# Kernel optimization log

Hardware: AMD Instinct MI355X
Metric: run time of the kernel (lower is better)

The kernel has to match this reference:

```python
import jax, jax.numpy as jnp
import numpy as np

N, E, IN, H, D = 50000, 800000, 16, 4, 64


def _gat_layer(x, W, a_s, a_d, b, src, dst, heads, concat):
    n = x.shape[0]
    h = (x @ W).reshape(n, heads, -1)                 # [N,H,D]
    es = jnp.einsum('nhd,hd->nh', h, a_s)             # alpha_src per node
    ed = jnp.einsum('nhd,hd->nh', h, a_d)             # alpha_dst per node
    e = jax.nn.leaky_relu(es[src] + ed[dst], 0.2)     # [E,H]
    # segment softmax over incoming edges of each dst node
    m = jax.ops.segment_max(e, dst, num_segments=n)
    ex = jnp.exp(e - m[dst])
    den = jax.ops.segment_sum(ex, dst, num_segments=n)
    alpha = ex / den[dst]                             # [E,H]
    out = jax.ops.segment_sum(h[src] * alpha[:, :, None], dst, num_segments=n)
    out = out.reshape(n, -1) if concat else out.mean(axis=1)
    return out + b


def setup_inputs() -> dict:
    key = jax.random.key(0)
    ks = jax.random.split(key, 16)
    x = jax.random.normal(ks[0], (N, IN), dtype=jnp.float32)
    edge_index = jax.random.randint(ks[1], (2, E), 0, N, dtype=jnp.int32)

    def lin(k, fi, fo):
        return jax.random.normal(k, (fi, fo), dtype=jnp.float32) / np.sqrt(fi)

    def att(k, heads, d):
        return jax.random.normal(k, (heads, d), dtype=jnp.float32) / np.sqrt(d)

    return dict(
        x=x, edge_index=edge_index,
        W1=lin(ks[2], IN, H * D), a1s=att(ks[3], H, D), a1d=att(ks[4], H, D),
        b1=jnp.zeros((H * D,), jnp.float32),
        W2=lin(ks[5], H * D, H * D), a2s=att(ks[6], H, D), a2d=att(ks[7], H, D),
        b2=jnp.zeros((H * D,), jnp.float32),
        W3=lin(ks[8], H * D, D), a3s=att(ks[9], 1, D), a3d=att(ks[10], 1, D),
        b3=jnp.zeros((D,), jnp.float32),
    )


def reference(x, edge_index, W1, a1s, a1d, b1, W2, a2s, a2d, b2, W3, a3s, a3d, b3):
    n = x.shape[0]
    loop = jnp.arange(n, dtype=edge_index.dtype)  # PyG GATConv adds self-loops
    src = jnp.concatenate([edge_index[0], loop])
    dst = jnp.concatenate([edge_index[1], loop])
    h = jax.nn.elu(_gat_layer(x, W1, a1s, a1d, b1, src, dst, H, True))
    h = jax.nn.elu(_gat_layer(h, W2, a2s, a2d, b2, src, dst, H, True))
    node_emb = _gat_layer(h, W3, a3s, a3d, b3, src, dst, 1, False)  # [N,64]
    graph_emb = node_emb.mean(axis=0, keepdims=True)                # [1,64]
    return node_emb, graph_emb
```

## Files before the change

kernel.cpp:

```cpp
#include <hip/hip_runtime.h>
#include <math.h>

#define NNODES 50000

typedef __attribute__((ext_vector_type(8))) short short8;
typedef __attribute__((ext_vector_type(4))) float f32x4;

__device__ __forceinline__ unsigned short f2bf(float f) {
    unsigned u = __float_as_uint(f);
    u += 0x7fffu + ((u >> 16) & 1);
    return (unsigned short)(u >> 16);
}
__device__ __forceinline__ float bf2f(unsigned short h) {
    return __uint_as_float(((unsigned)h) << 16);
}
__device__ __forceinline__ float bflo(unsigned u) { return __uint_as_float(u << 16); }
__device__ __forceinline__ float bfhi(unsigned u) { return __uint_as_float(u & 0xffff0000u); }

__global__ __launch_bounds__(256) void deg_count_kernel(const int* __restrict__ ei,
                                                        int* __restrict__ deg, int E) {
    int i = blockIdx.x * 256 + threadIdx.x;
    if (i < E) atomicAdd(&deg[ei[E + i]], 1);
}

__global__ __launch_bounds__(256) void scan_partial_kernel(const int* __restrict__ deg,
                                                           int* __restrict__ bsum, int N) {
    __shared__ int ls[256];
    int t = threadIdx.x;
    int i = blockIdx.x * 256 + t;
    ls[t] = (i < N) ? deg[i] + 1 : 0;
    __syncthreads();
    #pragma unroll
    for (int off = 128; off; off >>= 1) {
        if (t < off) ls[t] += ls[t + off];
        __syncthreads();
    }
    if (t == 0) bsum[blockIdx.x] = ls[0];
}

__global__ __launch_bounds__(256) void scan_blocks_kernel(const int* __restrict__ bsum,
                                                          int* __restrict__ boff,
                                                          int* __restrict__ rowptrN, int nblk) {
    __shared__ int ls[256];
    int t = threadIdx.x;
    int v = (t < nblk) ? bsum[t] : 0;
    ls[t] = v;
    __syncthreads();
    for (int off = 1; off < 256; off <<= 1) {
        int u = (t >= off) ? ls[t - off] : 0;
        __syncthreads();
        ls[t] += u;
        __syncthreads();
    }
    if (t < nblk) boff[t] = ls[t] - v;
    if (t == 255) *rowptrN = ls[255];
}

__global__ __launch_bounds__(256) void scan_final_kernel(const int* __restrict__ deg,
                                                         const int* __restrict__ boff,
                                                         int* __restrict__ rowptr,
                                                         int* __restrict__ fill, int N) {
    __shared__ int ls[256];
    int t = threadIdx.x;
    int i = blockIdx.x * 256 + t;
    int v = (i < N) ? deg[i] + 1 : 0;
    ls[t] = v;
    __syncthreads();
    for (int off = 1; off < 256; off <<= 1) {
        int u = (t >= off) ? ls[t - off] : 0;
        __syncthreads();
        ls[t] += u;
        __syncthreads();
    }
    if (i < N) {
        int e = boff[blockIdx.x] + ls[t] - v;
        rowptr[i] = e;
        fill[i] = e;
    }
}

__global__ __launch_bounds__(256) void scatter_kernel(const int* __restrict__ ei,
                                                      int* __restrict__ fill,
                                                      int* __restrict__ col, int E, int N) {
    int i = blockIdx.x * 256 + threadIdx.x;
    int total = E + N;
    if (i >= total) return;
    int s, d;
    if (i < E) { s = ei[i]; d = ei[E + i]; }
    else       { s = i - E; d = s; }
    int pos = atomicAdd(&fill[d], 1);
    col[pos] = s;
}

__global__ __launch_bounds__(256) void wprep_kernel(const float* __restrict__ W2,
                                                    const float* __restrict__ W3,
                                                    unsigned short* __restrict__ W2Th,
                                                    unsigned short* __restrict__ W2Tl,
                                                    unsigned short* __restrict__ W3Th,
                                                    unsigned short* __restrict__ W3Tl) {
    int b = blockIdx.x;
    if (b < 256) {
        int k = b, n = threadIdx.x;
        float w = W2[k * 256 + n];
        unsigned short h = f2bf(w);
        unsigned short l = f2bf(w - bf2f(h));
        W2Th[n * 256 + k] = h;
        W2Tl[n * 256 + k] = l;
    } else {
        int n = b - 256, k = threadIdx.x;
        float w = W3[k * 64 + n];
        unsigned short h = f2bf(w);
        unsigned short l = f2bf(w - bf2f(h));
        W3Th[n * 256 + k] = h;
        W3Tl[n * 256 + k] = l;
    }
}

#define LDK 40

__global__ __launch_bounds__(256) void gemm2_mfma_kernel(const unsigned short* __restrict__ Ahb,
                                                         const unsigned short* __restrict__ Alb,
                                                         const unsigned short* __restrict__ WTh,
                                                         const unsigned short* __restrict__ WTl,
                                                         unsigned short* __restrict__ Cb,
                                                         const float* __restrict__ as_,
                                                         const float* __restrict__ ad_,
                                                         float* __restrict__ es,
                                                         float* __restrict__ ed,
                                                         int M) {
    __shared__ __align__(16) unsigned short Ah[128][LDK], Al[128][LDK];
    __shared__ __align__(16) unsigned short Bh[128][LDK], Bl[128][LDK];
    int tid  = threadIdx.x;
    int lane = tid & 63, wave = tid >> 6;
    int wm = wave >> 1, wn = wave & 1;
    int bm = blockIdx.x * 128;
    int bn = blockIdx.y * 128;
    int c = lane & 15, q = lane >> 4;

    f32x4 acc[4][4] = {};

    for (int k0 = 0; k0 < 256; k0 += 32) {
        #pragma unroll
        for (int p = 0; p < 2; ++p) {
            int idx = p * 256 + tid;
            int r   = idx >> 2;
            int kc  = (idx & 3) * 8;
            int grow = bm + r;
            size_t go = (size_t)grow * 256 + k0 + kc;
            uint4 vh = make_uint4(0u,0u,0u,0u), vl = make_uint4(0u,0u,0u,0u);
            if (grow < M) {
                vh = *reinterpret_cast<const uint4*>(Ahb + go);
                vl = *reinterpret_cast<const uint4*>(Alb + go);
            }
            *reinterpret_cast<uint4*>(&Ah[r][kc]) = vh;
            *reinterpret_cast<uint4*>(&Al[r][kc]) = vl;
        }
        #pragma unroll
        for (int p = 0; p < 2; ++p) {
            int idx = p * 256 + tid;
            int n   = idx >> 2;
            int kc  = (idx & 3) * 8;
            const size_t go = (size_t)(bn + n) * 256 + k0 + kc;
            *reinterpret_cast<uint4*>(&Bh[n][kc]) = *reinterpret_cast<const uint4*>(WTh + go);
            *reinterpret_cast<uint4*>(&Bl[n][kc]) = *reinterpret_cast<const uint4*>(WTl + go);
        }
        __syncthreads();

        short8 bh[4], bl[4];
        #pragma unroll
        for (int nt = 0; nt < 4; ++nt) {
            bh[nt] = *reinterpret_cast<const short8*>(&Bh[wn * 64 + nt * 16 + c][q * 8]);
            bl[nt] = *reinterpret_cast<const short8*>(&Bl[wn * 64 + nt * 16 + c][q * 8]);
        }
        #pragma unroll
        for (int mt = 0; mt < 4; ++mt) {
            short8 ah = *reinterpret_cast<const short8*>(&Ah[wm * 64 + mt * 16 + c][q * 8]);
            short8 al = *reinterpret_cast<const short8*>(&Al[wm * 64 + mt * 16 + c][q * 8]);
            #pragma unroll
            for (int nt = 0; nt < 4; ++nt) {
                acc[mt][nt] = __builtin_amdgcn_mfma_f32_16x16x32_bf16(ah, bh[nt], acc[mt][nt], 0, 0, 0);
                acc[mt][nt] = __builtin_amdgcn_mfma_f32_16x16x32_bf16(ah, bl[nt], acc[mt][nt], 0, 0, 0);
                acc[mt][nt] = __builtin_amdgcn_mfma_f32_16x16x32_bf16(al, bh[nt], acc[mt][nt], 0, 0, 0);
            }
        }
        __syncthreads();
    }

    #pragma unroll
    for (int mt = 0; mt < 4; ++mt) {
        #pragma unroll
        for (int r = 0; r < 4; ++r) {
            int gr = bm + wm * 64 + mt * 16 + q * 4 + r;
            if (gr < M) {
                #pragma unroll
                for (int nt = 0; nt < 4; ++nt) {
                    Cb[(size_t)gr * 256 + bn + wn * 64 + nt * 16 + c] = f2bf(acc[mt][nt][r]);
                }
            }
        }
    }
    int head = blockIdx.y * 2 + wn;
    float asv[4], adv[4];
    #pragma unroll
    for (int nt = 0; nt < 4; ++nt) {
        asv[nt] = as_[head * 64 + nt * 16 + c];
        adv[nt] = ad_[head * 64 + nt * 16 + c];
    }
    #pragma unroll
    for (int mt = 0; mt < 4; ++mt) {
        #pragma unroll
        for (int r = 0; r < 4; ++r) {
            float s = 0.f, d = 0.f;
            #pragma unroll
            for (int nt = 0; nt < 4; ++nt) {
                s += acc[mt][nt][r] * asv[nt];
                d += acc[mt][nt][r] * adv[nt];
            }
            #pragma unroll
            for (int off = 1; off < 16; off <<= 1) {
                s += __shfl_xor(s, off, 64);
                d += __shfl_xor(d, off, 64);
            }
            int gr = bm + wm * 64 + mt * 16 + q * 4 + r;
            if (c == 0 && gr < M) {
                es[(size_t)gr * 4 + head] = s;
                ed[(size_t)gr * 4 + head] = d;
            }
        }
    }
}

__global__ __launch_bounds__(256) void gemm3_mfma_kernel(const unsigned short* __restrict__ Ab,
                                                         const unsigned short* __restrict__ WTh,
                                                         const unsigned short* __restrict__ WTl,
                                                         unsigned short* __restrict__ Cb,
                                                         const float* __restrict__ as_,
                                                         const float* __restrict__ ad_,
                                                         float* __restrict__ es,
                                                         float* __restrict__ ed,
                                                         int M) {
    __shared__ __align__(16) unsigned short Ah[128][LDK];
    __shared__ __align__(16) unsigned short Bh[64][LDK], Bl[64][LDK];
    int tid = threadIdx.x, lane = tid & 63, wave = tid >> 6;
    int bm = blockIdx.x * 128;
    int c = lane & 15, q = lane >> 4;
    f32x4 acc[2][4] = {};

    for (int k0 = 0; k0 < 256; k0 += 32) {
        #pragma unroll
        for (int p = 0; p < 2; ++p) {
            int idx = p * 256 + tid;
            int r   = idx >> 2;
            int kf  = (idx & 3) * 8;
            int grow = bm + r;
            uint4 v = (grow < M)
                ? *reinterpret_cast<const uint4*>(Ab + (size_t)grow * 256 + k0 + kf)
                : make_uint4(0u, 0u, 0u, 0u);
            *reinterpret_cast<uint4*>(&Ah[r][kf]) = v;
        }
        {
            int n  = tid >> 2;
            int kc = (tid & 3) * 8;
            size_t go = (size_t)n * 256 + k0 + kc;
            *reinterpret_cast<uint4*>(&Bh[n][kc]) = *reinterpret_cast<const uint4*>(WTh + go);
            *reinterpret_cast<uint4*>(&Bl[n][kc]) = *reinterpret_cast<const uint4*>(WTl + go);
        }
        __syncthreads();

        short8 bh[4], bl[4];
        #pragma unroll
        for (int nt = 0; nt < 4; ++nt) {
            bh[nt] = *reinterpret_cast<const short8*>(&Bh[nt * 16 + c][q * 8]);
            bl[nt] = *reinterpret_cast<const short8*>(&Bl[nt * 16 + c][q * 8]);
        }
        #pragma unroll
        for (int mt = 0; mt < 2; ++mt) {
            short8 a = *reinterpret_cast<const short8*>(&Ah[wave * 32 + mt * 16 + c][q * 8]);
            #pragma unroll
            for (int nt = 0; nt < 4; ++nt) {
                acc[mt][nt] = __builtin_amdgcn_mfma_f32_16x16x32_bf16(a, bh[nt], acc[mt][nt], 0, 0, 0);
                acc[mt][nt] = __builtin_amdgcn_mfma_f32_16x16x32_bf16(a, bl[nt], acc[mt][nt], 0, 0, 0);
            }
        }
        __syncthreads();
    }

    float asv[4], adv[4];
    #pragma unroll
    for (int nt = 0; nt < 4; ++nt) { asv[nt] = as_[nt * 16 + c]; adv[nt] = ad_[nt * 16 + c]; }
    #pragma unroll
    for (int mt = 0; mt < 2; ++mt) {
        #pragma unroll
        for (int r = 0; r < 4; ++r) {
            int gr = bm + wave * 32 + mt * 16 + q * 4 + r;
            bool ok = gr < M;
            if (ok) {
                #pragma unroll
                for (int nt = 0; nt < 4; ++nt)
                    Cb[(size_t)gr * 64 + nt * 16 + c] = f2bf(acc[mt][nt][r]);
            }
            float s = 0.f, d = 0.f;
            #pragma unroll
            for (int nt = 0; nt < 4; ++nt) {
                s += acc[mt][nt][r] * asv[nt];
                d += acc[mt][nt][r] * adv[nt];
            }
            #pragma unroll
            for (int off = 1; off < 16; off <<= 1) {
                s += __shfl_xor(s, off, 64);
                d += __shfl_xor(d, off, 64);
            }
            if (c == 0 && ok) { es[gr] = s; ed[gr] = d; }
        }
    }
}

template <int H>
__global__ __launch_bounds__(256) void gemm_attn_kernel(const float* __restrict__ A,
                                                        const float* __restrict__ B,
                                                        unsigned short* __restrict__ Cb,
                                                        const float* __restrict__ as_,
                                                        const float* __restrict__ ad_,
                                                        float* __restrict__ es,
                                                        float* __restrict__ ed,
                                                        int M, int K, int Ncol) {
    __shared__ __align__(16) float As[16][64];
    __shared__ __align__(16) float Bs[16][64];
    int tid = threadIdx.x;
    int bm = blockIdx.x * 64;
    int bn = blockIdx.y * 64;
    int tm = (tid >> 4) * 4;
    int tn = (tid & 15) * 4;
    float acc[4][4] = {};
    int ar  = tid >> 2;
    int akk = (tid & 3) * 4;
    int brr = tid >> 4;
    int bcc = (tid & 15) * 4;
    for (int k0 = 0; k0 < K; k0 += 16) {
        int grow = bm + ar;
        float4 av;
        if (grow < M) av = *reinterpret_cast<const float4*>(A + (size_t)grow * K + k0 + akk);
        else          av = make_float4(0.f, 0.f, 0.f, 0.f);
        As[akk + 0][ar] = av.x;
        As[akk + 1][ar] = av.y;
        As[akk + 2][ar] = av.z;
        As[akk + 3][ar] = av.w;
        float4 bv = *reinterpret_cast<const float4*>(B + (size_t)(k0 + brr) * Ncol + bn + bcc);
        *reinterpret_cast<float4*>(&Bs[brr][bcc]) = bv;
        __syncthreads();
        #pragma unroll
        for (int kk = 0; kk < 16; ++kk) {
            float4 a4 = *reinterpret_cast<const float4*>(&As[kk][tm]);
            float4 b4 = *reinterpret_cast<const float4*>(&Bs[kk][tn]);
            float a[4] = {a4.x, a4.y, a4.z, a4.w};
            float b[4] = {b4.x, b4.y, b4.z, b4.w};
            #pragma unroll
            for (int i = 0; i < 4; ++i)
                #pragma unroll
                for (int j = 0; j < 4; ++j) acc[i][j] += a[i] * b[j];
        }
        __syncthreads();
    }
    #pragma unroll
    for (int i = 0; i < 4; ++i) {
        int gr = bm + tm + i;
        if (gr < M) {
            ushort4 r;
            r.x = f2bf(acc[i][0]); r.y = f2bf(acc[i][1]);
            r.z = f2bf(acc[i][2]); r.w = f2bf(acc[i][3]);
            *reinterpret_cast<ushort4*>(Cb + (size_t)gr * Ncol + bn + tn) = r;
        }
    }
    int hy = blockIdx.y;
    float4 asv = *reinterpret_cast<const float4*>(as_ + (size_t)hy * 64 + tn);
    float4 adv = *reinterpret_cast<const float4*>(ad_ + (size_t)hy * 64 + tn);
    float sv[4], dv[4];
    #pragma unroll
    for (int i = 0; i < 4; ++i) {
        sv[i] = acc[i][0] * asv.x + acc[i][1] * asv.y + acc[i][2] * asv.z + acc[i][3] * asv.w;
        dv[i] = acc[i][0] * adv.x + acc[i][1] * adv.y + acc[i][2] * adv.z + acc[i][3] * adv.w;
    }
    #pragma unroll
    for (int off = 1; off < 16; off <<= 1) {
        #pragma unroll
        for (int i = 0; i < 4; ++i) {
            sv[i] += __shfl_xor(sv[i], off, 64);
            dv[i] += __shfl_xor(dv[i], off, 64);
        }
    }
    if ((tid & 15) == 0) {
        #pragma unroll
        for (int i = 0; i < 4; ++i) {
            int gr = bm + tm + i;
            if (gr < M) {
                es[(size_t)gr * H + hy] = sv[i];
                ed[(size_t)gr * H + hy] = dv[i];
            }
        }
    }
}

__device__ __forceinline__ float lrelu02(float x) { return x > 0.f ? x : 0.2f * x; }
__device__ __forceinline__ float eluf(float x)    { return x > 0.f ? x : expm1f(x); }

template <int ACT, int OUTMODE>
__global__ __launch_bounds__(256) void agg4_kernel(const unsigned short* __restrict__ hb,
                                                   const float* __restrict__ es,
                                                   const float* __restrict__ ed,
                                                   const int* __restrict__ rowptr,
                                                   const int* __restrict__ col,
                                                   const float* __restrict__ bias,
                                                   void* __restrict__ outp,
                                                   void* __restrict__ outp2, int N) {
    __shared__ uint2 spds[4][4][66];
    int sub  = threadIdx.x >> 6;
    int lane = threadIdx.x & 63;
    int node = blockIdx.x * 4 + sub;
    if (node >= N) return;
    int s = rowptr[node], t = rowptr[node + 1];

    float edv[4];
    #pragma unroll
    for (int h = 0; h < 4; ++h) edv[h] = ed[(size_t)node * 4 + h];

    int hh = lane >> 4;
    float den = 0.f;
    float4 acc = make_float4(0.f, 0.f, 0.f, 0.f);
    for (int base = s; base < t; base += 64) {
        int j = base + lane;
        int m = t - base; if (m > 64) m = 64;
        int sc = 0;
        float p[4] = {0.f, 0.f, 0.f, 0.f};
        if (j < t) {
            sc = col[j];
            float4 e4 = *reinterpret_cast<const float4*>(es + (size_t)sc * 4);
            p[0] = __expf(lrelu02(e4.x + edv[0]));
            p[1] = __expf(lrelu02(e4.y + edv[1]));
            p[2] = __expf(lrelu02(e4.z + edv[2]));
            p[3] = __expf(lrelu02(e4.w + edv[3]));
        }
        #pragma unroll
        for (int h = 0; h < 4; ++h)
            spds[sub][h][lane] = make_uint2((unsigned)sc, __float_as_uint(p[h]));
        #pragma unroll 4
        for (int jj = 0; jj < m; ++jj) {
            uint2 sp = spds[sub][hh][jj];
            float a = __uint_as_float(sp.y);
            den += a;
            uint2 u = *reinterpret_cast<const uint2*>(hb + (size_t)sp.x * 256 + lane * 4);
            acc.x += bflo(u.x) * a;
            acc.y += bfhi(u.x) * a;
            acc.z += bflo(u.y) * a;
            acc.w += bfhi(u.y) * a;
        }
    }
    float inv = 1.f / den;
    float4 bv = *reinterpret_cast<const float4*>(bias + lane * 4);
    float r0 = acc.x * inv + bv.x;
    float r1 = acc.y * inv + bv.y;
    float r2 = acc.z * inv + bv.z;
    float r3 = acc.w * inv + bv.w;
    if (ACT) { r0 = eluf(r0); r1 = eluf(r1); r2 = eluf(r2); r3 = eluf(r3); }
    if constexpr (OUTMODE == 0) {
        *reinterpret_cast<float4*>((float*)outp + (size_t)node * 256 + lane * 4) =
            make_float4(r0, r1, r2, r3);
    } else if constexpr (OUTMODE == 1) {
        ushort4 o;
        o.x = f2bf(r0); o.y = f2bf(r1); o.z = f2bf(r2); o.w = f2bf(r3);
        *reinterpret_cast<ushort4*>((unsigned short*)outp + (size_t)node * 256 + lane * 4) = o;
    } else {
        ushort4 oh, ol;
        oh.x = f2bf(r0); ol.x = f2bf(r0 - bf2f(oh.x));
        oh.y = f2bf(r1); ol.y = f2bf(r1 - bf2f(oh.y));
        oh.z = f2bf(r2); ol.z = f2bf(r2 - bf2f(oh.z));
        oh.w = f2bf(r3); ol.w = f2bf(r3 - bf2f(oh.w));
        size_t o = (size_t)node * 256 + lane * 4;
        *reinterpret_cast<ushort4*>((unsigned short*)outp  + o) = oh;
        *reinterpret_cast<ushort4*>((unsigned short*)outp2 + o) = ol;
    }
}

__global__ __launch_bounds__(256) void agg1_kernel(const unsigned short* __restrict__ hb,
                                                   const float* __restrict__ es,
                                                   const float* __restrict__ ed,
                                                   const int* __restrict__ rowptr,
                                                   const int* __restrict__ col,
                                                   const float* __restrict__ bias,
                                                   float* __restrict__ out, int N) {
    __shared__ uint2 spds[4][66];
    int sub  = threadIdx.x >> 6;
    int lane = threadIdx.x & 63;
    int node = blockIdx.x * 4 + sub;
    if (node >= N) return;
    int s = rowptr[node], t = rowptr[node + 1];
    float edv = ed[node];

    int half = lane >> 5, sl = lane & 31;
    float den = 0.f, acc0 = 0.f, acc1 = 0.f;
    for (int base = s; base < t; base += 64) {
        int j = base + lane;
        int m = t - base; if (m > 64) m = 64;
        int sc = 0;
        float p0 = 0.f;
        if (j < t) {
            sc = col[j];
            p0 = __expf(lrelu02(es[sc] + edv));
        }
        spds[sub][lane] = make_uint2((unsigned)sc, __float_as_uint(p0));
        int nit = (m + 1) >> 1;
        #pragma unroll 4
        for (int it = 0; it < nit; ++it) {
            int idx = 2 * it + half;
            uint2 sp = spds[sub][idx];
            float a = __uint_as_float(sp.y);
            den += a;
            unsigned u = *reinterpret_cast<const unsigned*>(hb + (size_t)sp.x * 64 + sl * 2);
            acc0 += bflo(u) * a;
            acc1 += bfhi(u) * a;
        }
    }
    acc0 += __shfl_xor(acc0, 32, 64);
    acc1 += __shfl_xor(acc1, 32, 64);
    den  += __shfl_xor(den, 32, 64);
    if (half == 0) {
        float inv = 1.f / den;
        float2 b = *reinterpret_cast<const float2*>(bias + sl * 2);
        *reinterpret_cast<float2*>(out + (size_t)node * 64 + sl * 2) =
            make_float2(acc0 * inv + b.x, acc1 * inv + b.y);
    }
}

__global__ __launch_bounds__(256) void gmean_partial(const float* __restrict__ ne,
                                                     float* __restrict__ part, int N) {
    int d = threadIdx.x & 63, sub = threadIdx.x >> 6;
    int start = blockIdx.x * 4 + sub;
    float s = 0.f;
    for (int n = start; n < N; n += gridDim.x * 4) s += ne[(size_t)n * 64 + d];
    __shared__ float ls[256];
    ls[threadIdx.x] = s;
    __syncthreads();
    if (threadIdx.x < 64) {
        float v = ls[threadIdx.x] + ls[threadIdx.x + 64] + ls[threadIdx.x + 128] + ls[threadIdx.x + 192];
        part[blockIdx.x * 64 + d] = v;
    }
}

__global__ __launch_bounds__(64) void gmean_final(const float* __restrict__ part,
                                                  float* __restrict__ gout, int nblk, float invN) {
    int d = threadIdx.x;
    float s = 0.f;
    for (int b = 0; b < nblk; ++b) s += part[b * 64 + d];
    gout[d] = s * invN;
}

extern "C" void kernel_launch(void* const* d_in, const int* in_sizes, int n_in,
                              void* d_out, int out_size, void* d_ws, size_t ws_size,
                              hipStream_t stream) {
    const float* x   = (const float*)d_in[0];
    const int*   ei  = (const int*)d_in[1];
    const float* W1  = (const float*)d_in[2];
    const float* a1s = (const float*)d_in[3];
    const float* a1d = (const float*)d_in[4];
    const float* b1  = (const float*)d_in[5];
    const float* W2  = (const float*)d_in[6];
    const float* a2s = (const float*)d_in[7];
    const float* a2d = (const float*)d_in[8];
    const float* b2  = (const float*)d_in[9];
    const float* W3  = (const float*)d_in[10];
    const float* a3s = (const float*)d_in[11];
    const float* a3d = (const float*)d_in[12];
    const float* b3  = (const float*)d_in[13];
    float* out = (float*)d_out;

    const int N = NNODES;
    const int E = in_sizes[1] / 2;
    const int NB = (N + 255) / 256;

    char* w = (char*)d_ws;
    unsigned short* Hb   = (unsigned short*)w; w += (size_t)N * 256 * 2;
    unsigned short* B0b  = (unsigned short*)w; w += (size_t)N * 256 * 2;
    unsigned short* H3b  = (unsigned short*)w; w += (size_t)N * 64 * 2;
    unsigned short* A1h  = (unsigned short*)w; w += (size_t)N * 256 * 2;
    unsigned short* A1l  = (unsigned short*)w; w += (size_t)N * 256 * 2;
    float* es = (float*)w; w += (size_t)N * 4 * 4;
    float* ed = (float*)w; w += (size_t)N * 4 * 4;
    unsigned short* W2Th = (unsigned short*)w; w += 256 * 256 * 2;
    unsigned short* W2Tl = (unsigned short*)w; w += 256 * 256 * 2;
    unsigned short* W3Th = (unsigned short*)w; w += 64 * 256 * 2;
    unsigned short* W3Tl = (unsigned short*)w; w += 64 * 256 * 2;
    int* deg    = (int*)w; w += (size_t)N * 4;
    int* rowptr = (int*)w; w += (size_t)(N + 2) * 4;
    int* fill   = (int*)w; w += (size_t)N * 4;
    int* col    = (int*)w; w += (size_t)(E + N) * 4;
    int* bsum   = (int*)w; w += 256 * 4;
    int* boff   = (int*)w; w += 256 * 4;
    float* part = (float*)w; w += 128 * 64 * 4;
    (void)ws_size; (void)n_in; (void)out_size;

    hipMemsetAsync(deg, 0, (size_t)N * 4, stream);
    deg_count_kernel<<<(E + 255) / 256, 256, 0, stream>>>(ei, deg, E);
    scan_partial_kernel<<<NB, 256, 0, stream>>>(deg, bsum, N);
    scan_blocks_kernel<<<1, 256, 0, stream>>>(bsum, boff, rowptr + N, NB);
    scan_final_kernel<<<NB, 256, 0, stream>>>(deg, boff, rowptr, fill, N);
    scatter_kernel<<<(E + N + 255) / 256, 256, 0, stream>>>(ei, fill, col, E, N);
    wprep_kernel<<<320, 256, 0, stream>>>(W2, W3, W2Th, W2Tl, W3Th, W3Tl);

    gemm_attn_kernel<4><<<dim3((N + 63) / 64, 4), 256, 0, stream>>>(
        x, W1, Hb, a1s, a1d, es, ed, N, 16, 256);
    agg4_kernel<1, 2><<<(N + 3) / 4, 256, 0, stream>>>(Hb, es, ed, rowptr, col, b1, A1h, A1l, N);

    gemm2_mfma_kernel<<<dim3((N + 127) / 128, 2), 256, 0, stream>>>(
        A1h, A1l, W2Th, W2Tl, Hb, a2s, a2d, es, ed, N);
    agg4_kernel<1, 1><<<(N + 3) / 4, 256, 0, stream>>>(Hb, es, ed, rowptr, col, b2, B0b, nullptr, N);

    gemm3_mfma_kernel<<<(N + 127) / 128, 256, 0, stream>>>(
        B0b, W3Th, W3Tl, H3b, a3s, a3d, es, ed, N);
    agg1_kernel<<<(N + 3) / 4, 256, 0, stream>>>(H3b, es, ed, rowptr, col, b3, out, N);

    gmean_partial<<<128, 256, 0, stream>>>(out, part, N);
    gmean_final<<<1, 64, 0, stream>>>(part, out + (size_t)N * 64, 128, 1.0f / N);
}
```

Before: 457.2 us.

## Aggregate raw 16-dim inputs before the first-layer projection

```diff
diff --git a/kernel.cpp b/kernel.cpp
--- a/kernel.cpp
+++ b/kernel.cpp
@@ -92,12 +92,17 @@
     col[pos] = s;
 }
 
-__global__ __launch_bounds__(256) void wprep_kernel(const float* __restrict__ W2,
+__global__ __launch_bounds__(256) void wprep_kernel(const float* __restrict__ W1,
+                                                    const float* __restrict__ a1s,
+                                                    const float* __restrict__ a1d,
+                                                    const float* __restrict__ W2,
                                                     const float* __restrict__ W3,
                                                     unsigned short* __restrict__ W2Th,
                                                     unsigned short* __restrict__ W2Tl,
                                                     unsigned short* __restrict__ W3Th,
-                                                    unsigned short* __restrict__ W3Tl) {
+                                                    unsigned short* __restrict__ W3Tl,
+                                                    float* __restrict__ w1s,
+                                                    float* __restrict__ w1d) {
     int b = blockIdx.x;
     if (b < 256) {
         int k = b, n = threadIdx.x;
@@ -106,13 +111,181 @@
         unsigned short l = f2bf(w - bf2f(h));
         W2Th[n * 256 + k] = h;
         W2Tl[n * 256 + k] = l;
-    } else {
+    } else if (b < 320) {
         int n = b - 256, k = threadIdx.x;
         float w = W3[k * 64 + n];
         unsigned short h = f2bf(w);
         unsigned short l = f2bf(w - bf2f(h));
         W3Th[n * 256 + k] = h;
         W3Tl[n * 256 + k] = l;
+    } else {
+        int t = threadIdx.x;
+        if (t < 128) {
+            int which = t >> 6;
+            int hk = t & 63;
+            int h = hk >> 4, k = hk & 15;
+            const float* av = which ? a1d : a1s;
+            float s = 0.f;
+            for (int d = 0; d < 64; ++d)
+                s += W1[k * 256 + h * 64 + d] * av[h * 64 + d];
+            (which ? w1d : w1s)[hk] = s;
+        }
+    }
+}
+
+__global__ __launch_bounds__(256) void esed1_kernel(const float* __restrict__ x,
+                                                    const float* __restrict__ w1s,
+                                                    const float* __restrict__ w1d,
+                                                    float* __restrict__ es,
+                                                    float* __restrict__ ed, int N) {
+    int i = blockIdx.x * 256 + threadIdx.x;
+    if (i >= N) return;
+    float xv[16];
+    #pragma unroll
+    for (int p = 0; p < 4; ++p) {
+        float4 v = *reinterpret_cast<const float4*>(x + (size_t)i * 16 + p * 4);
+        xv[p * 4 + 0] = v.x; xv[p * 4 + 1] = v.y; xv[p * 4 + 2] = v.z; xv[p * 4 + 3] = v.w;
+    }
+    float4 se, de;
+    float* sp = &se.x; float* dp = &de.x;
+    #pragma unroll
+    for (int h = 0; h < 4; ++h) {
+        float s = 0.f, d = 0.f;
+        #pragma unroll
+        for (int k = 0; k < 16; ++k) {
+            s += xv[k] * w1s[h * 16 + k];
+            d += xv[k] * w1d[h * 16 + k];
+        }
+        sp[h] = s; dp[h] = d;
+    }
+    *reinterpret_cast<float4*>(es + (size_t)i * 4) = se;
+    *reinterpret_cast<float4*>(ed + (size_t)i * 4) = de;
+}
+
+__device__ __forceinline__ float lrelu02(float x) { return x > 0.f ? x : 0.2f * x; }
+__device__ __forceinline__ float eluf(float x)    { return x > 0.f ? x : expm1f(x); }
+
+__global__ __launch_bounds__(256) void aggx_kernel(const float* __restrict__ x,
+                                                   const float* __restrict__ es,
+                                                   const float* __restrict__ ed,
+                                                   const int* __restrict__ rowptr,
+                                                   const int* __restrict__ col,
+                                                   float* __restrict__ zn, int N) {
+    __shared__ int    slds[4][64];
+    __shared__ float4 plds[4][64];
+    int sub  = threadIdx.x >> 6;
+    int lane = threadIdx.x & 63;
+    int node = blockIdx.x * 4 + sub;
+    if (node >= N) return;
+    int s = rowptr[node], t = rowptr[node + 1];
+
+    float edv[4];
+    #pragma unroll
+    for (int h = 0; h < 4; ++h) edv[h] = ed[(size_t)node * 4 + h];
+
+    int eg = lane >> 4, d = lane & 15;
+    float acc[4] = {0.f, 0.f, 0.f, 0.f};
+    float den[4] = {0.f, 0.f, 0.f, 0.f};
+
+    for (int base = s; base < t; base += 64) {
+        int j = base + lane;
+        int m = t - base; if (m > 64) m = 64;
+        int sc = 0;
+        float4 p = make_float4(0.f, 0.f, 0.f, 0.f);
+        if (j < t) {
+            sc = col[j];
+            float4 e4 = *reinterpret_cast<const float4*>(es + (size_t)sc * 4);
+            p.x = __expf(lrelu02(e4.x + edv[0]));
+            p.y = __expf(lrelu02(e4.y + edv[1]));
+            p.z = __expf(lrelu02(e4.z + edv[2]));
+            p.w = __expf(lrelu02(e4.w + edv[3]));
+        }
+        slds[sub][lane] = sc;
+        plds[sub][lane] = p;
+        int nit = (m + 3) >> 2;
+        #pragma unroll 4
+        for (int it = 0; it < nit; ++it) {
+            int e = it * 4 + eg;
+            int scj = slds[sub][e];
+            float4 pj = plds[sub][e];
+            float xv = x[(size_t)scj * 16 + d];
+            acc[0] += pj.x * xv; acc[1] += pj.y * xv;
+            acc[2] += pj.z * xv; acc[3] += pj.w * xv;
+            den[0] += pj.x; den[1] += pj.y; den[2] += pj.z; den[3] += pj.w;
+        }
+    }
+    #pragma unroll
+    for (int h = 0; h < 4; ++h) {
+        acc[h] += __shfl_xor(acc[h], 16, 64);
+        acc[h] += __shfl_xor(acc[h], 32, 64);
+        den[h] += __shfl_xor(den[h], 16, 64);
+        den[h] += __shfl_xor(den[h], 32, 64);
+    }
+    float a = (eg == 0) ? acc[0] : (eg == 1) ? acc[1] : (eg == 2) ? acc[2] : acc[3];
+    float dn = (eg == 0) ? den[0] : (eg == 1) ? den[1] : (eg == 2) ? den[2] : den[3];
+    zn[(size_t)node * 64 + lane] = a / dn;
+}
+
+__global__ __launch_bounds__(256) void gemm1z_kernel(const float* __restrict__ zn,
+                                                     const float* __restrict__ W1,
+                                                     const float* __restrict__ b1,
+                                                     unsigned short* __restrict__ A1h,
+                                                     unsigned short* __restrict__ A1l,
+                                                     int M) {
+    __shared__ __align__(16) float As[16][64];
+    __shared__ __align__(16) float Bs[16][64];
+    int tid = threadIdx.x;
+    int bm = blockIdx.x * 64;
+    int hy = blockIdx.y;
+    int tm = (tid >> 4) * 4;
+    int tn = (tid & 15) * 4;
+    float acc[4][4] = {};
+    int ar  = tid >> 2;
+    int akk = (tid & 3) * 4;
+    int brr = tid >> 4;
+    int bcc = (tid & 15) * 4;
+    {
+        int grow = bm + ar;
+        float4 av = (grow < M)
+            ? *reinterpret_cast<const float4*>(zn + (size_t)grow * 64 + hy * 16 + akk)
+            : make_float4(0.f, 0.f, 0.f, 0.f);
+        As[akk + 0][ar] = av.x;
+        As[akk + 1][ar] = av.y;
+        As[akk + 2][ar] = av.z;
+        As[akk + 3][ar] = av.w;
+        float4 bv = *reinterpret_cast<const float4*>(W1 + (size_t)brr * 256 + hy * 64 + bcc);
+        *reinterpret_cast<float4*>(&Bs[brr][bcc]) = bv;
+        __syncthreads();
+        #pragma unroll
+        for (int kk = 0; kk < 16; ++kk) {
+            float4 a4 = *reinterpret_cast<const float4*>(&As[kk][tm]);
+            float4 b4 = *reinterpret_cast<const float4*>(&Bs[kk][tn]);
+            float a[4] = {a4.x, a4.y, a4.z, a4.w};
+            float b[4] = {b4.x, b4.y, b4.z, b4.w};
+            #pragma unroll
+            for (int i = 0; i < 4; ++i)
+                #pragma unroll
+                for (int j = 0; j < 4; ++j) acc[i][j] += a[i] * b[j];
+        }
+    }
+    float4 bb = *reinterpret_cast<const float4*>(b1 + hy * 64 + tn);
+    #pragma unroll
+    for (int i = 0; i < 4; ++i) {
+        int gr = bm + tm + i;
+        if (gr < M) {
+            float r0 = eluf(acc[i][0] + bb.x);
+            float r1 = eluf(acc[i][1] + bb.y);
+            float r2 = eluf(acc[i][2] + bb.z);
+            float r3 = eluf(acc[i][3] + bb.w);
+            ushort4 oh, ol;
+            oh.x = f2bf(r0); ol.x = f2bf(r0 - bf2f(oh.x));
+            oh.y = f2bf(r1); ol.y = f2bf(r1 - bf2f(oh.y));
+            oh.z = f2bf(r2); ol.z = f2bf(r2 - bf2f(oh.z));
+            oh.w = f2bf(r3); ol.w = f2bf(r3 - bf2f(oh.w));
+            size_t o = (size_t)gr * 256 + hy * 64 + tn;
+            *reinterpret_cast<ushort4*>(A1h + o) = oh;
+            *reinterpret_cast<ushort4*>(A1l + o) = ol;
+        }
     }
 }
 
@@ -314,94 +487,6 @@
         }
     }
 }
-
-template <int H>
-__global__ __launch_bounds__(256) void gemm_attn_kernel(const float* __restrict__ A,
-                                                        const float* __restrict__ B,
-                                                        unsigned short* __restrict__ Cb,
-                                                        const float* __restrict__ as_,
-                                                        const float* __restrict__ ad_,
-                                                        float* __restrict__ es,
-                                                        float* __restrict__ ed,
-                                                        int M, int K, int Ncol) {
-    __shared__ __align__(16) float As[16][64];
-    __shared__ __align__(16) float Bs[16][64];
-    int tid = threadIdx.x;
-    int bm = blockIdx.x * 64;
-    int bn = blockIdx.y * 64;
-    int tm = (tid >> 4) * 4;
-    int tn = (tid & 15) * 4;
-    float acc[4][4] = {};
-    int ar  = tid >> 2;
-    int akk = (tid & 3) * 4;
-    int brr = tid >> 4;
-    int bcc = (tid & 15) * 4;
-    for (int k0 = 0; k0 < K; k0 += 16) {
-        int grow = bm + ar;
-        float4 av;
-        if (grow < M) av = *reinterpret_cast<const float4*>(A + (size_t)grow * K + k0 + akk);
-        else          av = make_float4(0.f, 0.f, 0.f, 0.f);
-        As[akk + 0][ar] = av.x;
-        As[akk + 1][ar] = av.y;
-        As[akk + 2][ar] = av.z;
-        As[akk + 3][ar] = av.w;
-        float4 bv = *reinterpret_cast<const float4*>(B + (size_t)(k0 + brr) * Ncol + bn + bcc);
-        *reinterpret_cast<float4*>(&Bs[brr][bcc]) = bv;
-        __syncthreads();
-        #pragma unroll
-        for (int kk = 0; kk < 16; ++kk) {
-            float4 a4 = *reinterpret_cast<const float4*>(&As[kk][tm]);
-            float4 b4 = *reinterpret_cast<const float4*>(&Bs[kk][tn]);
-            float a[4] = {a4.x, a4.y, a4.z, a4.w};
-            float b[4] = {b4.x, b4.y, b4.z, b4.w};
-            #pragma unroll
-            for (int i = 0; i < 4; ++i)
-                #pragma unroll
-                for (int j = 0; j < 4; ++j) acc[i][j] += a[i] * b[j];
-        }
-        __syncthreads();
-    }
-    #pragma unroll
-    for (int i = 0; i < 4; ++i) {
-        int gr = bm + tm + i;
-        if (gr < M) {
-            ushort4 r;
-            r.x = f2bf(acc[i][0]); r.y = f2bf(acc[i][1]);
-            r.z = f2bf(acc[i][2]); r.w = f2bf(acc[i][3]);
-            *reinterpret_cast<ushort4*>(Cb + (size_t)gr * Ncol + bn + tn) = r;
-        }
-    }
-    int hy = blockIdx.y;
-    float4 asv = *reinterpret_cast<const float4*>(as_ + (size_t)hy * 64 + tn);
-    float4 adv = *reinterpret_cast<const float4*>(ad_ + (size_t)hy * 64 + tn);
-    float sv[4], dv[4];
-    #pragma unroll
-    for (int i = 0; i < 4; ++i) {
-        sv[i] = acc[i][0] * asv.x + acc[i][1] * asv.y + acc[i][2] * asv.z + acc[i][3] * asv.w;
-        dv[i] = acc[i][0] * adv.x + acc[i][1] * adv.y + acc[i][2] * adv.z + acc[i][3] * adv.w;
-    }
-    #pragma unroll
-    for (int off = 1; off < 16; off <<= 1) {
-        #pragma unroll
-        for (int i = 0; i < 4; ++i) {
-            sv[i] += __shfl_xor(sv[i], off, 64);
-            dv[i] += __shfl_xor(dv[i], off, 64);
-        }
-    }
-    if ((tid & 15) == 0) {
-        #pragma unroll
-        for (int i = 0; i < 4; ++i) {
-            int gr = bm + tm + i;
-            if (gr < M) {
-                es[(size_t)gr * H + hy] = sv[i];
-                ed[(size_t)gr * H + hy] = dv[i];
-            }
-        }
-    }
-}
-
-__device__ __forceinline__ float lrelu02(float x) { return x > 0.f ? x : 0.2f * x; }
-__device__ __forceinline__ float eluf(float x)    { return x > 0.f ? x : expm1f(x); }
 
 template <int ACT, int OUTMODE>
 __global__ __launch_bounds__(256) void agg4_kernel(const unsigned short* __restrict__ hb,
@@ -582,12 +667,15 @@
     unsigned short* H3b  = (unsigned short*)w; w += (size_t)N * 64 * 2;
     unsigned short* A1h  = (unsigned short*)w; w += (size_t)N * 256 * 2;
     unsigned short* A1l  = (unsigned short*)w; w += (size_t)N * 256 * 2;
+    float* zn = (float*)w; w += (size_t)N * 64 * 4;
     float* es = (float*)w; w += (size_t)N * 4 * 4;
     float* ed = (float*)w; w += (size_t)N * 4 * 4;
     unsigned short* W2Th = (unsigned short*)w; w += 256 * 256 * 2;
     unsigned short* W2Tl = (unsigned short*)w; w += 256 * 256 * 2;
     unsigned short* W3Th = (unsigned short*)w; w += 64 * 256 * 2;
     unsigned short* W3Tl = (unsigned short*)w; w += 64 * 256 * 2;
+    float* w1s = (float*)w; w += 64 * 4;
+    float* w1d = (float*)w; w += 64 * 4;
     int* deg    = (int*)w; w += (size_t)N * 4;
     int* rowptr = (int*)w; w += (size_t)(N + 2) * 4;
     int* fill   = (int*)w; w += (size_t)N * 4;
@@ -603,11 +691,12 @@
     scan_blocks_kernel<<<1, 256, 0, stream>>>(bsum, boff, rowptr + N, NB);
     scan_final_kernel<<<NB, 256, 0, stream>>>(deg, boff, rowptr, fill, N);
     scatter_kernel<<<(E + N + 255) / 256, 256, 0, stream>>>(ei, fill, col, E, N);
-    wprep_kernel<<<320, 256, 0, stream>>>(W2, W3, W2Th, W2Tl, W3Th, W3Tl);
-
-    gemm_attn_kernel<4><<<dim3((N + 63) / 64, 4), 256, 0, stream>>>(
-        x, W1, Hb, a1s, a1d, es, ed, N, 16, 256);
-    agg4_kernel<1, 2><<<(N + 3) / 4, 256, 0, stream>>>(Hb, es, ed, rowptr, col, b1, A1h, A1l, N);
+    wprep_kernel<<<321, 256, 0, stream>>>(W1, a1s, a1d, W2, W3,
+                                          W2Th, W2Tl, W3Th, W3Tl, w1s, w1d);
+
+    esed1_kernel<<<NB, 256, 0, stream>>>(x, w1s, w1d, es, ed, N);
+    aggx_kernel<<<(N + 3) / 4, 256, 0, stream>>>(x, es, ed, rowptr, col, zn, N);
+    gemm1z_kernel<<<dim3((N + 63) / 64, 4), 256, 0, stream>>>(zn, W1, b1, A1h, A1l, N);
 
     gemm2_mfma_kernel<<<dim3((N + 127) / 128, 2), 256, 0, stream>>>(
         A1h, A1l, W2Th, W2Tl, Hb, a2s, a2d, es, ed, N);
```

Result: faster. 428.5 us (-6.3%).
